# Performance work log

Measured on AMD Instinct MI355X. Metric: run time of the kernel, lower is better.

The kernel has to match this reference:

```python
import jax, jax.numpy as jnp
import numpy as np

N_NODES = 100000
N_EDGES = 800000
N_FEAT = 128
N_HID = 128
N_LAYERS = 3
N_CLASSES = 10
N_GRAPHS = 256


def setup_inputs() -> dict:
    key = jax.random.key(0)
    ks = jax.random.split(key, 6)
    x = jax.random.normal(ks[0], (N_NODES, N_FEAT), dtype=jnp.float32)
    edge_index = jax.random.randint(ks[1], (2, N_EDGES), 0, N_NODES, dtype=jnp.int64)
    batch = jnp.sort(jax.random.randint(ks[2], (N_NODES,), 0, N_GRAPHS, dtype=jnp.int64))
    # GCNConv weights: layer 0 is [num_feature, num_hidden], rest [hid, hid];
    # num_feature == num_hidden here so we stack them as [L, H, H].
    Ws = jax.random.normal(ks[3], (N_LAYERS, N_HID, N_HID), dtype=jnp.float32) * 0.05
    bs = jnp.zeros((N_LAYERS, N_HID), dtype=jnp.float32)
    Wc = jax.random.normal(ks[4], (N_HID, N_CLASSES), dtype=jnp.float32) * 0.05
    bc = jnp.zeros((N_CLASSES,), dtype=jnp.float32)
    return {"x": x, "edge_index": edge_index, "batch": batch,
            "Ws": Ws, "bs": bs, "Wc": Wc, "bc": bc}


def reference(x, edge_index, batch, Ws, bs, Wc, bc):
    n = x.shape[0]
    # PyG GCNConv: add self-loops, symmetric normalization deg^{-1/2} A deg^{-1/2}
    loop = jnp.arange(n, dtype=edge_index.dtype)
    src = jnp.concatenate([edge_index[0], loop])  # [E+N]
    dst = jnp.concatenate([edge_index[1], loop])
    deg = jax.ops.segment_sum(jnp.ones_like(src, dtype=x.dtype), dst, num_segments=n)
    dinv = jax.lax.rsqrt(deg)  # deg >= 1 due to self-loops
    norm = dinv[src] * dinv[dst]  # [E+N]

    for l in range(N_LAYERS):
        h = x @ Ws[l]  # [N, H] dense transform
        msgs = h[src] * norm[:, None]  # gather + scale, [E+N, H]
        x = jax.ops.segment_sum(msgs, dst, num_segments=n) + bs[l]
        x = jax.nn.elu(x)
        # F.dropout(training=self.training): identity in eval mode

    g = jax.ops.segment_max(x, batch, num_segments=N_GRAPHS)  # global_max_pool [G, H]
    logits = g @ Wc + bc
    return jax.nn.softmax(logits, axis=1)
```

## Files before the change

kernel.cpp:

```cpp
#include <hip/hip_runtime.h>
#include <float.h>
#include <math.h>

#define NNODES 100000
#define NEDGES 800000
#define NF 128
#define NCLASSES 10
#define NGRAPHS 256

#define NBIN 98
#define BCHUNK 4096
#define NB2 196
#define CNTS_PAD 20480
#define SCAN_CHUNK 2048

typedef __attribute__((ext_vector_type(8))) short bf16x8;
typedef __attribute__((ext_vector_type(4))) float f32x4;

__device__ inline ushort f2bf(float f) {
    unsigned u = __float_as_uint(f);
    u = u + 0x7FFFu + ((u >> 16) & 1u);
    return (ushort)(u >> 16);
}
__device__ inline float b2f(ushort h) {
    return __uint_as_float(((unsigned)h) << 16);
}
__device__ inline void up2(unsigned u, float& lo, float& hi) {
    lo = __uint_as_float(u << 16);
    hi = __uint_as_float(u & 0xFFFF0000u);
}
__device__ inline unsigned fenc(float f) {
    unsigned u = __float_as_uint(f);
    return ((int)u < 0) ? ~u : (u | 0x80000000u);
}
__device__ inline float fdec(unsigned s) {
    return (s & 0x80000000u) ? __uint_as_float(s ^ 0x80000000u) : __uint_as_float(~s);
}

__global__ __launch_bounds__(256) void binct_kernel(const int* __restrict__ dst,
                                                    unsigned* __restrict__ cnts, int E) {
    __shared__ unsigned lh[NBIN];
    int tid = threadIdx.x;
    if (tid < NBIN) lh[tid] = 0;
    __syncthreads();
    int e0 = blockIdx.x * BCHUNK;
    int e1 = min(e0 + BCHUNK, E);
    for (int e = e0 + tid; e < e1; e += 256)
        atomicAdd(&lh[dst[e] >> 10], 1u);
    __syncthreads();
    if (tid < NBIN) cnts[tid * NB2 + blockIdx.x] = lh[tid];
}

__global__ __launch_bounds__(256) void scanA_kernel(const unsigned* __restrict__ cnt,
                                                    unsigned* __restrict__ bsum, int N) {
    __shared__ unsigned wsum[4];
    int tid = threadIdx.x, wid = tid >> 6, lane = tid & 63;
    int base = blockIdx.x * SCAN_CHUNK + tid * 8;
    unsigned s = 0;
    if (base < N) {
        uint4 a = *(const uint4*)(cnt + base);
        uint4 b = *(const uint4*)(cnt + base + 4);
        s = a.x + a.y + a.z + a.w + b.x + b.y + b.z + b.w;
    }
    #pragma unroll
    for (int off = 32; off >= 1; off >>= 1) s += __shfl_down(s, off, 64);
    if (lane == 0) wsum[wid] = s;
    __syncthreads();
    if (tid == 0) bsum[blockIdx.x] = wsum[0] + wsum[1] + wsum[2] + wsum[3];
}

__global__ __launch_bounds__(64) void scanB_kernel(const unsigned* __restrict__ bsum,
                                                   unsigned* __restrict__ boff, int nb) {
    int lane = threadIdx.x;
    unsigned v = (lane < nb) ? bsum[lane] : 0u;
    unsigned incl = v;
    #pragma unroll
    for (int off = 1; off < 64; off <<= 1) {
        unsigned t = __shfl_up(incl, off, 64);
        if (lane >= off) incl += t;
    }
    if (lane < nb) boff[lane] = incl - v;
}

__global__ __launch_bounds__(256) void scanC_kernel(const unsigned* __restrict__ cnt,
                                                    const unsigned* __restrict__ boff,
                                                    unsigned* __restrict__ outp, int N) {
    __shared__ unsigned wsum[4];
    int tid = threadIdx.x, wid = tid >> 6, lane = tid & 63;
    int base = blockIdx.x * SCAN_CHUNK + tid * 8;
    unsigned v[8];
    unsigned s = 0;
    bool act = base < N;
    if (act) {
        uint4 a = *(const uint4*)(cnt + base);
        uint4 b = *(const uint4*)(cnt + base + 4);
        v[0] = a.x; v[1] = a.y; v[2] = a.z; v[3] = a.w;
        v[4] = b.x; v[5] = b.y; v[6] = b.z; v[7] = b.w;
        #pragma unroll
        for (int j = 0; j < 8; ++j) s += v[j];
    }
    unsigned incl = s;
    #pragma unroll
    for (int off = 1; off < 64; off <<= 1) {
        unsigned t = __shfl_up(incl, off, 64);
        if (lane >= off) incl += t;
    }
    if (lane == 63) wsum[wid] = incl;
    __syncthreads();
    unsigned woff = 0;
    for (int w = 0; w < 4; ++w) if (w < wid) woff += wsum[w];
    if (act) {
        unsigned run = incl - s + woff + boff[blockIdx.x];
        #pragma unroll
        for (int j = 0; j < 8; ++j) {
            outp[base + j] = run;
            run += v[j];
        }
    }
}

__global__ __launch_bounds__(256) void binscatter_kernel(const int* __restrict__ src,
                                                         const int* __restrict__ dst,
                                                         const unsigned* __restrict__ offs,
                                                         unsigned* __restrict__ bedge, int E) {
    __shared__ unsigned lcur[NBIN];
    int tid = threadIdx.x;
    if (tid < NBIN) lcur[tid] = offs[tid * NB2 + blockIdx.x];
    __syncthreads();
    int e0 = blockIdx.x * BCHUNK;
    int e1 = min(e0 + BCHUNK, E);
    for (int e = e0 + tid; e < e1; e += 256) {
        int d = dst[e];
        int b = d >> 10;
        unsigned pos = atomicAdd(&lcur[b], 1u);
        bedge[pos] = ((unsigned)src[e] << 10) | (unsigned)(d & 1023);
    }
}

__global__ __launch_bounds__(256) void bucket_kernel(const unsigned* __restrict__ bedge,
                                                     const unsigned* __restrict__ offs,
                                                     float* __restrict__ dinv,
                                                     unsigned* __restrict__ rowptr,
                                                     unsigned* __restrict__ csr_src, int N) {
    __shared__ unsigned lcnt[1024];
    __shared__ unsigned lcur[1024];
    __shared__ unsigned wsum[4];
    int b = blockIdx.x;
    int tid = threadIdx.x, wid = tid >> 6, lane = tid & 63;
    unsigned ebeg = offs[b * NB2], eend = offs[(b + 1) * NB2];
    lcnt[tid] = 0; lcnt[tid + 256] = 0; lcnt[tid + 512] = 0; lcnt[tid + 768] = 0;
    __syncthreads();
    for (unsigned e = ebeg + tid; e < eend; e += 256)
        atomicAdd(&lcnt[bedge[e] & 1023], 1u);
    __syncthreads();
    unsigned c[4];
    unsigned s = 0;
    #pragma unroll
    for (int j = 0; j < 4; ++j) { c[j] = lcnt[tid * 4 + j]; s += c[j]; }
    unsigned incl = s;
    #pragma unroll
    for (int off = 1; off < 64; off <<= 1) {
        unsigned t = __shfl_up(incl, off, 64);
        if (lane >= off) incl += t;
    }
    if (lane == 63) wsum[wid] = incl;
    __syncthreads();
    unsigned woff = 0;
    for (int w = 0; w < 4; ++w) if (w < wid) woff += wsum[w];
    unsigned run = (incl - s) + woff + ebeg;
    int gbase = b * 1024 + tid * 4;
    #pragma unroll
    for (int j = 0; j < 4; ++j) {
        if (gbase + j < N) {
            rowptr[gbase + j] = run;
            dinv[gbase + j] = rsqrtf((float)c[j] + 1.0f);
        }
        lcur[tid * 4 + j] = run;
        run += c[j];
    }
    if (b == NBIN - 1 && tid == 0) rowptr[N] = eend;
    __syncthreads();
    for (unsigned e = ebeg + tid; e < eend; e += 256) {
        unsigned v = bedge[e];
        unsigned pos = atomicAdd(&lcur[v & 1023], 1u);
        csr_src[pos] = v >> 10;
    }
}

__global__ __launch_bounds__(256) void wprep_kernel(const float* __restrict__ Ws,
                                                    short* __restrict__ Wf) {
    int l = blockIdx.x;
    for (int idx = threadIdx.x; idx < 16384; idx += 256) {
        int i = idx & 7;
        int lane = (idx >> 3) & 63;
        int ns = idx >> 9;
        int s = ns & 3, nt = ns >> 2;
        int k = s * 32 + (lane >> 4) * 8 + i;
        int n = nt * 16 + (lane & 15);
        Wf[l * 16384 + idx] = (short)f2bf(Ws[l * 16384 + k * NF + n]);
    }
}

template<bool L0>
__global__ __launch_bounds__(256) void gemm_mfma_kernel(const void* __restrict__ Xin,
                                                        const short* __restrict__ Wf,
                                                        ushort* __restrict__ Hb, int M) {
    __shared__ short Wl[16384];
    int tid = threadIdx.x;
    for (int i = tid; i < 2048; i += 256)
        ((float4*)Wl)[i] = ((const float4*)Wf)[i];

    int wave = tid >> 6, lane = tid & 63;
    int r = lane & 15, kg = lane >> 4;
    int rowbase = blockIdx.x * 128 + wave * 32;

    bf16x8 afrag[2][4];
    #pragma unroll
    for (int t = 0; t < 2; ++t) {
        #pragma unroll
        for (int s = 0; s < 4; ++s) {
            int row = rowbase + t * 16 + r;
            if (row > M - 1) row = M - 1;
            if (L0) {
                const float* p = (const float*)Xin + (size_t)row * NF + s * 32 + kg * 8;
                float4 u0 = *(const float4*)p;
                float4 u1 = *(const float4*)(p + 4);
                bf16x8 a;
                a[0] = (short)f2bf(u0.x); a[1] = (short)f2bf(u0.y);
                a[2] = (short)f2bf(u0.z); a[3] = (short)f2bf(u0.w);
                a[4] = (short)f2bf(u1.x); a[5] = (short)f2bf(u1.y);
                a[6] = (short)f2bf(u1.z); a[7] = (short)f2bf(u1.w);
                afrag[t][s] = a;
            } else {
                afrag[t][s] = *(const bf16x8*)((const ushort*)Xin + (size_t)row * NF + s * 32 + kg * 8);
            }
        }
    }

    f32x4 acc[2][8];
    #pragma unroll
    for (int t = 0; t < 2; ++t)
        #pragma unroll
        for (int n = 0; n < 8; ++n)
            acc[t][n] = (f32x4){0.f, 0.f, 0.f, 0.f};

    __syncthreads();
    const bf16x8* WL = (const bf16x8*)Wl;
    #pragma unroll
    for (int s = 0; s < 4; ++s) {
        #pragma unroll
        for (int n = 0; n < 8; ++n) {
            bf16x8 bfr = WL[(n * 4 + s) * 64 + lane];
            acc[0][n] = __builtin_amdgcn_mfma_f32_16x16x32_bf16(afrag[0][s], bfr, acc[0][n], 0, 0, 0);
            acc[1][n] = __builtin_amdgcn_mfma_f32_16x16x32_bf16(afrag[1][s], bfr, acc[1][n], 0, 0, 0);
        }
    }

    __syncthreads();
    ushort* Cl = (ushort*)Wl;
    int r4 = kg * 4;
    #pragma unroll
    for (int t = 0; t < 2; ++t) {
        #pragma unroll
        for (int n = 0; n < 8; ++n) {
            #pragma unroll
            for (int q = 0; q < 4; ++q) {
                Cl[(wave * 32 + t * 16 + r4 + q) * NF + n * 16 + r] = f2bf(acc[t][n][q]);
            }
        }
    }
    __syncthreads();
    int row0 = blockIdx.x * 128;
    #pragma unroll
    for (int k = 0; k < 8; ++k) {
        int c = k * 256 + tid;
        int row = row0 + (c >> 4);
        if (row < M)
            ((uint4*)Hb)[(size_t)row * 16 + (c & 15)] = ((const uint4*)Cl)[c];
    }
}

__global__ __launch_bounds__(256) void aggregate_kernel(const ushort* __restrict__ Hb,
                                                        const float* __restrict__ dinv,
                                                        const unsigned* __restrict__ rowptr,
                                                        const unsigned* __restrict__ csr_src,
                                                        const float* __restrict__ bias,
                                                        ushort* __restrict__ Xout, int N) {
    int gid = blockIdx.x * 256 + threadIdx.x;
    int node = gid >> 4;
    int lane = gid & 15;
    int c0 = lane * 8;
    float di = dinv[node];
    float sl = di * di;
    float4 b0 = ((const float4*)bias)[lane * 2 + 0];
    float4 b1 = ((const float4*)bias)[lane * 2 + 1];
    uint4 hv = *(const uint4*)(Hb + (size_t)node * NF + c0);
    float a0, a1, a2, a3, a4, a5, a6, a7, t0, t1;
    up2(hv.x, t0, t1); a0 = fmaf(t0, sl, b0.x); a1 = fmaf(t1, sl, b0.y);
    up2(hv.y, t0, t1); a2 = fmaf(t0, sl, b0.z); a3 = fmaf(t1, sl, b0.w);
    up2(hv.z, t0, t1); a4 = fmaf(t0, sl, b1.x); a5 = fmaf(t1, sl, b1.y);
    up2(hv.w, t0, t1); a6 = fmaf(t0, sl, b1.z); a7 = fmaf(t1, sl, b1.w);
    unsigned e = rowptr[node], end = rowptr[node + 1];
    for (; e + 4 <= end; e += 4) {
        unsigned s0 = csr_src[e + 0], s1 = csr_src[e + 1];
        unsigned s2 = csr_src[e + 2], s3 = csr_src[e + 3];
        float n0 = dinv[s0] * di, n1 = dinv[s1] * di;
        float n2 = dinv[s2] * di, n3 = dinv[s3] * di;
        uint4 g0 = *(const uint4*)(Hb + (size_t)s0 * NF + c0);
        uint4 g1 = *(const uint4*)(Hb + (size_t)s1 * NF + c0);
        uint4 g2 = *(const uint4*)(Hb + (size_t)s2 * NF + c0);
        uint4 g3 = *(const uint4*)(Hb + (size_t)s3 * NF + c0);
        up2(g0.x, t0, t1); a0 = fmaf(t0, n0, a0); a1 = fmaf(t1, n0, a1);
        up2(g0.y, t0, t1); a2 = fmaf(t0, n0, a2); a3 = fmaf(t1, n0, a3);
        up2(g0.z, t0, t1); a4 = fmaf(t0, n0, a4); a5 = fmaf(t1, n0, a5);
        up2(g0.w, t0, t1); a6 = fmaf(t0, n0, a6); a7 = fmaf(t1, n0, a7);
        up2(g1.x, t0, t1); a0 = fmaf(t0, n1, a0); a1 = fmaf(t1, n1, a1);
        up2(g1.y, t0, t1); a2 = fmaf(t0, n1, a2); a3 = fmaf(t1, n1, a3);
        up2(g1.z, t0, t1); a4 = fmaf(t0, n1, a4); a5 = fmaf(t1, n1, a5);
        up2(g1.w, t0, t1); a6 = fmaf(t0, n1, a6); a7 = fmaf(t1, n1, a7);
        up2(g2.x, t0, t1); a0 = fmaf(t0, n2, a0); a1 = fmaf(t1, n2, a1);
        up2(g2.y, t0, t1); a2 = fmaf(t0, n2, a2); a3 = fmaf(t1, n2, a3);
        up2(g2.z, t0, t1); a4 = fmaf(t0, n2, a4); a5 = fmaf(t1, n2, a5);
        up2(g2.w, t0, t1); a6 = fmaf(t0, n2, a6); a7 = fmaf(t1, n2, a7);
        up2(g3.x, t0, t1); a0 = fmaf(t0, n3, a0); a1 = fmaf(t1, n3, a1);
        up2(g3.y, t0, t1); a2 = fmaf(t0, n3, a2); a3 = fmaf(t1, n3, a3);
        up2(g3.z, t0, t1); a4 = fmaf(t0, n3, a4); a5 = fmaf(t1, n3, a5);
        up2(g3.w, t0, t1); a6 = fmaf(t0, n3, a6); a7 = fmaf(t1, n3, a7);
    }
    for (; e < end; ++e) {
        unsigned s = csr_src[e];
        float nm = dinv[s] * di;
        uint4 g = *(const uint4*)(Hb + (size_t)s * NF + c0);
        up2(g.x, t0, t1); a0 = fmaf(t0, nm, a0); a1 = fmaf(t1, nm, a1);
        up2(g.y, t0, t1); a2 = fmaf(t0, nm, a2); a3 = fmaf(t1, nm, a3);
        up2(g.z, t0, t1); a4 = fmaf(t0, nm, a4); a5 = fmaf(t1, nm, a5);
        up2(g.w, t0, t1); a6 = fmaf(t0, nm, a6); a7 = fmaf(t1, nm, a7);
    }
    a0 = a0 > 0.f ? a0 : expm1f(a0);
    a1 = a1 > 0.f ? a1 : expm1f(a1);
    a2 = a2 > 0.f ? a2 : expm1f(a2);
    a3 = a3 > 0.f ? a3 : expm1f(a3);
    a4 = a4 > 0.f ? a4 : expm1f(a4);
    a5 = a5 > 0.f ? a5 : expm1f(a5);
    a6 = a6 > 0.f ? a6 : expm1f(a6);
    a7 = a7 > 0.f ? a7 : expm1f(a7);
    uint4 o;
    o.x = ((unsigned)f2bf(a1) << 16) | f2bf(a0);
    o.y = ((unsigned)f2bf(a3) << 16) | f2bf(a2);
    o.z = ((unsigned)f2bf(a5) << 16) | f2bf(a4);
    o.w = ((unsigned)f2bf(a7) << 16) | f2bf(a6);
    *(uint4*)(Xout + (size_t)node * NF + c0) = o;
}

__global__ __launch_bounds__(256) void aggregate_pool_kernel(const ushort* __restrict__ Hb,
                                                             const float* __restrict__ dinv,
                                                             const unsigned* __restrict__ rowptr,
                                                             const unsigned* __restrict__ csr_src,
                                                             const float* __restrict__ bias,
                                                             const int* __restrict__ batch,
                                                             unsigned* __restrict__ Gx, int N) {
    __shared__ unsigned lmax[16][NF];
    __shared__ int g0s;
    int tid = threadIdx.x;
    int gid = blockIdx.x * 256 + tid;
    int node = gid >> 4;
    int lane = gid & 15;
    int c0 = lane * 8;
    for (int i = tid; i < 16 * NF; i += 256) ((unsigned*)lmax)[i] = 0;
    if (tid == 0) g0s = batch[blockIdx.x * 16];
    __syncthreads();
    float di = dinv[node];
    float sl = di * di;
    float4 b0 = ((const float4*)bias)[lane * 2 + 0];
    float4 b1 = ((const float4*)bias)[lane * 2 + 1];
    uint4 hv = *(const uint4*)(Hb + (size_t)node * NF + c0);
    float a0, a1, a2, a3, a4, a5, a6, a7, t0, t1;
    up2(hv.x, t0, t1); a0 = fmaf(t0, sl, b0.x); a1 = fmaf(t1, sl, b0.y);
    up2(hv.y, t0, t1); a2 = fmaf(t0, sl, b0.z); a3 = fmaf(t1, sl, b0.w);
    up2(hv.z, t0, t1); a4 = fmaf(t0, sl, b1.x); a5 = fmaf(t1, sl, b1.y);
    up2(hv.w, t0, t1); a6 = fmaf(t0, sl, b1.z); a7 = fmaf(t1, sl, b1.w);
    unsigned e = rowptr[node], end = rowptr[node + 1];
    for (; e + 4 <= end; e += 4) {
        unsigned s0 = csr_src[e + 0], s1 = csr_src[e + 1];
        unsigned s2 = csr_src[e + 2], s3 = csr_src[e + 3];
        float n0 = dinv[s0] * di, n1 = dinv[s1] * di;
        float n2 = dinv[s2] * di, n3 = dinv[s3] * di;
        uint4 g0 = *(const uint4*)(Hb + (size_t)s0 * NF + c0);
        uint4 g1 = *(const uint4*)(Hb + (size_t)s1 * NF + c0);
        uint4 g2 = *(const uint4*)(Hb + (size_t)s2 * NF + c0);
        uint4 g3 = *(const uint4*)(Hb + (size_t)s3 * NF + c0);
        up2(g0.x, t0, t1); a0 = fmaf(t0, n0, a0); a1 = fmaf(t1, n0, a1);
        up2(g0.y, t0, t1); a2 = fmaf(t0, n0, a2); a3 = fmaf(t1, n0, a3);
        up2(g0.z, t0, t1); a4 = fmaf(t0, n0, a4); a5 = fmaf(t1, n0, a5);
        up2(g0.w, t0, t1); a6 = fmaf(t0, n0, a6); a7 = fmaf(t1, n0, a7);
        up2(g1.x, t0, t1); a0 = fmaf(t0, n1, a0); a1 = fmaf(t1, n1, a1);
        up2(g1.y, t0, t1); a2 = fmaf(t0, n1, a2); a3 = fmaf(t1, n1, a3);
        up2(g1.z, t0, t1); a4 = fmaf(t0, n1, a4); a5 = fmaf(t1, n1, a5);
        up2(g1.w, t0, t1); a6 = fmaf(t0, n1, a6); a7 = fmaf(t1, n1, a7);
        up2(g2.x, t0, t1); a0 = fmaf(t0, n2, a0); a1 = fmaf(t1, n2, a1);
        up2(g2.y, t0, t1); a2 = fmaf(t0, n2, a2); a3 = fmaf(t1, n2, a3);
        up2(g2.z, t0, t1); a4 = fmaf(t0, n2, a4); a5 = fmaf(t1, n2, a5);
        up2(g2.w, t0, t1); a6 = fmaf(t0, n2, a6); a7 = fmaf(t1, n2, a7);
        up2(g3.x, t0, t1); a0 = fmaf(t0, n3, a0); a1 = fmaf(t1, n3, a1);
        up2(g3.y, t0, t1); a2 = fmaf(t0, n3, a2); a3 = fmaf(t1, n3, a3);
        up2(g3.z, t0, t1); a4 = fmaf(t0, n3, a4); a5 = fmaf(t1, n3, a5);
        up2(g3.w, t0, t1); a6 = fmaf(t0, n3, a6); a7 = fmaf(t1, n3, a7);
    }
    for (; e < end; ++e) {
        unsigned s = csr_src[e];
        float nm = dinv[s] * di;
        uint4 g = *(const uint4*)(Hb + (size_t)s * NF + c0);
        up2(g.x, t0, t1); a0 = fmaf(t0, nm, a0); a1 = fmaf(t1, nm, a1);
        up2(g.y, t0, t1); a2 = fmaf(t0, nm, a2); a3 = fmaf(t1, nm, a3);
        up2(g.z, t0, t1); a4 = fmaf(t0, nm, a4); a5 = fmaf(t1, nm, a5);
        up2(g.w, t0, t1); a6 = fmaf(t0, nm, a6); a7 = fmaf(t1, nm, a7);
    }
    a0 = a0 > 0.f ? a0 : expm1f(a0);
    a1 = a1 > 0.f ? a1 : expm1f(a1);
    a2 = a2 > 0.f ? a2 : expm1f(a2);
    a3 = a3 > 0.f ? a3 : expm1f(a3);
    a4 = a4 > 0.f ? a4 : expm1f(a4);
    a5 = a5 > 0.f ? a5 : expm1f(a5);
    a6 = a6 > 0.f ? a6 : expm1f(a6);
    a7 = a7 > 0.f ? a7 : expm1f(a7);
    int slot = batch[node] - g0s;
    unsigned* lm = &lmax[slot][c0];
    atomicMax(lm + 0, fenc(a0)); atomicMax(lm + 1, fenc(a1));
    atomicMax(lm + 2, fenc(a2)); atomicMax(lm + 3, fenc(a3));
    atomicMax(lm + 4, fenc(a4)); atomicMax(lm + 5, fenc(a5));
    atomicMax(lm + 6, fenc(a6)); atomicMax(lm + 7, fenc(a7));
    __syncthreads();
    for (int i = tid; i < 16 * NF; i += 256) {
        unsigned v = ((unsigned*)lmax)[i];
        if (v) atomicMax(&Gx[(size_t)(g0s + (i >> 7)) * NF + (i & (NF - 1))], v);
    }
}

__global__ __launch_bounds__(128) void classify_kernel(const unsigned* __restrict__ Gx,
                                                       const float* __restrict__ Wc,
                                                       const float* __restrict__ bc,
                                                       float* __restrict__ out) {
    __shared__ float gr[NF];
    __shared__ float lg[NCLASSES];
    int g = blockIdx.x;
    int tid = threadIdx.x;
    gr[tid] = fdec(Gx[(size_t)g * NF + tid]);
    __syncthreads();
    if (tid < NCLASSES) {
        float s = bc[tid];
        for (int k = 0; k < NF; ++k) s = fmaf(gr[k], Wc[k * NCLASSES + tid], s);
        lg[tid] = s;
    }
    __syncthreads();
    if (tid == 0) {
        float m = lg[0];
        #pragma unroll
        for (int c = 1; c < NCLASSES; ++c) m = fmaxf(m, lg[c]);
        float e[NCLASSES];
        float sum = 0.f;
        #pragma unroll
        for (int c = 0; c < NCLASSES; ++c) { e[c] = expf(lg[c] - m); sum += e[c]; }
        #pragma unroll
        for (int c = 0; c < NCLASSES; ++c) out[g * NCLASSES + c] = e[c] / sum;
    }
}

extern "C" void kernel_launch(void* const* d_in, const int* in_sizes, int n_in,
                              void* d_out, int out_size, void* d_ws, size_t ws_size,
                              hipStream_t stream) {
    const float* x     = (const float*)d_in[0];
    const int*   ei    = (const int*)d_in[1];
    const int*   batch = (const int*)d_in[2];
    const float* Ws    = (const float*)d_in[3];
    const float* bs    = (const float*)d_in[4];
    const float* Wc    = (const float*)d_in[5];
    const float* bc    = (const float*)d_in[6];
    float* out = (float*)d_out;

    const int* src = ei;
    const int* dst = ei + NEDGES;

    char* ws = (char*)d_ws;
    size_t off = 0;
    auto alloc = [&](size_t bytes) -> void* {
        off = (off + 255) & ~(size_t)255;
        void* p = ws + off;
        off += bytes;
        return p;
    };
    ushort*   B0      = (ushort*)alloc(sizeof(ushort) * (size_t)NNODES * NF);
    ushort*   B1      = (ushort*)alloc(sizeof(ushort) * (size_t)NNODES * NF);
    ushort*   Hb      = (ushort*)alloc(sizeof(ushort) * (size_t)NNODES * NF);
    float*    dinvp   = (float*)alloc(sizeof(float) * NNODES);
    unsigned* rowptr  = (unsigned*)alloc(sizeof(unsigned) * (NNODES + 1));
    unsigned* csr_src = (unsigned*)alloc(sizeof(unsigned) * NEDGES);
    unsigned* bedge   = (unsigned*)alloc(sizeof(unsigned) * NEDGES);
    unsigned* offs    = (unsigned*)alloc(sizeof(unsigned) * (CNTS_PAD + 1));
    unsigned* bsum    = (unsigned*)alloc(sizeof(unsigned) * 16);
    unsigned* boff    = (unsigned*)alloc(sizeof(unsigned) * 16);
    short*    Wf      = (short*)alloc(sizeof(short) * 3 * 16384);
    unsigned* cnts    = (unsigned*)alloc(sizeof(unsigned) * CNTS_PAD);
    unsigned* Gx      = (unsigned*)alloc(sizeof(unsigned) * NGRAPHS * NF);
    size_t zspan = (size_t)((char*)(Gx + NGRAPHS * NF) - (char*)cnts);

    hipMemsetAsync(cnts, 0, zspan, stream);
    wprep_kernel<<<3, 256, 0, stream>>>(Ws, Wf);
    binct_kernel<<<NB2, 256, 0, stream>>>(dst, cnts, NEDGES);
    scanA_kernel<<<CNTS_PAD / SCAN_CHUNK, 256, 0, stream>>>(cnts, bsum, CNTS_PAD);
    scanB_kernel<<<1, 64, 0, stream>>>(bsum, boff, CNTS_PAD / SCAN_CHUNK);
    scanC_kernel<<<CNTS_PAD / SCAN_CHUNK, 256, 0, stream>>>(cnts, boff, offs, CNTS_PAD);
    binscatter_kernel<<<NB2, 256, 0, stream>>>(src, dst, offs, bedge, NEDGES);
    bucket_kernel<<<NBIN, 256, 0, stream>>>(bedge, offs, dinvp, rowptr, csr_src, NNODES);

    int gemm_grid = (NNODES + 127) / 128;
    int agg_grid  = NNODES / 16;

    gemm_mfma_kernel<true><<<gemm_grid, 256, 0, stream>>>(x, Wf + 0 * 16384, Hb, NNODES);
    aggregate_kernel<<<agg_grid, 256, 0, stream>>>(Hb, dinvp, rowptr, csr_src,
                                                   bs + 0 * NF, B1, NNODES);
    gemm_mfma_kernel<false><<<gemm_grid, 256, 0, stream>>>(B1, Wf + 1 * 16384, Hb, NNODES);
    aggregate_kernel<<<agg_grid, 256, 0, stream>>>(Hb, dinvp, rowptr, csr_src,
                                                   bs + 1 * NF, B0, NNODES);
    gemm_mfma_kernel<false><<<gemm_grid, 256, 0, stream>>>(B0, Wf + 2 * 16384, Hb, NNODES);
    aggregate_pool_kernel<<<agg_grid, 256, 0, stream>>>(Hb, dinvp, rowptr, csr_src,
                                                        bs + 2 * NF, batch, Gx, NNODES);

    classify_kernel<<<NGRAPHS, 128, 0, stream>>>(Gx, Wc, bc, out);
}
```

Before: 232.2 us.

## Fuse aggregation with next layer's GEMM via shared-memory staging

Merges the aggregate kernel for layers 0 and 1 with the following MFMA GEMM into one 512-thread kernel. Each block aggregates 128 nodes into an XOR-swizzled LDS tile and then multiplies it by the next weight matrix, so the intermediate activation buffers are no longer written to and re-read from global memory. This also removes two kernel launches. In exchange the larger LDS footprint (about 64 KB per block) may lower occupancy, and the gather latency now sits in the same block as the GEMM phase.

```diff
diff --git a/kernel.cpp b/kernel.cpp
--- a/kernel.cpp
+++ b/kernel.cpp
@@ -201,10 +201,9 @@
     }
 }
 
-template<bool L0>
-__global__ __launch_bounds__(256) void gemm_mfma_kernel(const void* __restrict__ Xin,
-                                                        const short* __restrict__ Wf,
-                                                        ushort* __restrict__ Hb, int M) {
+__global__ __launch_bounds__(256) void gemm_l0_kernel(const float* __restrict__ Xin,
+                                                      const short* __restrict__ Wf,
+                                                      ushort* __restrict__ Hb, int M) {
     __shared__ short Wl[16384];
     int tid = threadIdx.x;
     for (int i = tid; i < 2048; i += 256)
@@ -221,19 +220,15 @@
         for (int s = 0; s < 4; ++s) {
             int row = rowbase + t * 16 + r;
             if (row > M - 1) row = M - 1;
-            if (L0) {
-                const float* p = (const float*)Xin + (size_t)row * NF + s * 32 + kg * 8;
-                float4 u0 = *(const float4*)p;
-                float4 u1 = *(const float4*)(p + 4);
-                bf16x8 a;
-                a[0] = (short)f2bf(u0.x); a[1] = (short)f2bf(u0.y);
-                a[2] = (short)f2bf(u0.z); a[3] = (short)f2bf(u0.w);
-                a[4] = (short)f2bf(u1.x); a[5] = (short)f2bf(u1.y);
-                a[6] = (short)f2bf(u1.z); a[7] = (short)f2bf(u1.w);
-                afrag[t][s] = a;
-            } else {
-                afrag[t][s] = *(const bf16x8*)((const ushort*)Xin + (size_t)row * NF + s * 32 + kg * 8);
-            }
+            const float* p = Xin + (size_t)row * NF + s * 32 + kg * 8;
+            float4 u0 = *(const float4*)p;
+            float4 u1 = *(const float4*)(p + 4);
+            bf16x8 a;
+            a[0] = (short)f2bf(u0.x); a[1] = (short)f2bf(u0.y);
+            a[2] = (short)f2bf(u0.z); a[3] = (short)f2bf(u0.w);
+            a[4] = (short)f2bf(u1.x); a[5] = (short)f2bf(u1.y);
+            a[6] = (short)f2bf(u1.z); a[7] = (short)f2bf(u1.w);
+            afrag[t][s] = a;
         }
     }
 
@@ -280,16 +275,150 @@
     }
 }
 
-__global__ __launch_bounds__(256) void aggregate_kernel(const ushort* __restrict__ Hb,
-                                                        const float* __restrict__ dinv,
-                                                        const unsigned* __restrict__ rowptr,
-                                                        const unsigned* __restrict__ csr_src,
-                                                        const float* __restrict__ bias,
-                                                        ushort* __restrict__ Xout, int N) {
-    int gid = blockIdx.x * 256 + threadIdx.x;
+__global__ __launch_bounds__(512) void fused_agg_gemm_kernel(const ushort* __restrict__ Hin,
+                                                             const float* __restrict__ dinv,
+                                                             const unsigned* __restrict__ rowptr,
+                                                             const unsigned* __restrict__ csr_src,
+                                                             const float* __restrict__ bias,
+                                                             const short* __restrict__ Wf,
+                                                             ushort* __restrict__ Hout, int M) {
+    __shared__ short Wl[16384];
+    __shared__ uint4 Xl4[128][16];
+
+    int tid = threadIdx.x;
+    for (int i = tid; i < 2048; i += 512)
+        ((float4*)Wl)[i] = ((const float4*)Wf)[i];
+
+    int lane16 = tid & 15;
+    int c0 = lane16 * 8;
+    float4 b0 = ((const float4*)bias)[lane16 * 2 + 0];
+    float4 b1 = ((const float4*)bias)[lane16 * 2 + 1];
+    #pragma unroll
+    for (int it = 0; it < 4; ++it) {
+        int row = it * 32 + (tid >> 4);
+        int node = blockIdx.x * 128 + row;
+        uint4 o = make_uint4(0u, 0u, 0u, 0u);
+        if (node < M) {
+            float di = dinv[node];
+            float sl = di * di;
+            uint4 hv = *(const uint4*)(Hin + (size_t)node * NF + c0);
+            float a0, a1, a2, a3, a4, a5, a6, a7, t0, t1;
+            up2(hv.x, t0, t1); a0 = fmaf(t0, sl, b0.x); a1 = fmaf(t1, sl, b0.y);
+            up2(hv.y, t0, t1); a2 = fmaf(t0, sl, b0.z); a3 = fmaf(t1, sl, b0.w);
+            up2(hv.z, t0, t1); a4 = fmaf(t0, sl, b1.x); a5 = fmaf(t1, sl, b1.y);
+            up2(hv.w, t0, t1); a6 = fmaf(t0, sl, b1.z); a7 = fmaf(t1, sl, b1.w);
+            unsigned e = rowptr[node], end = rowptr[node + 1];
+            for (; e + 4 <= end; e += 4) {
+                unsigned s0 = csr_src[e + 0], s1 = csr_src[e + 1];
+                unsigned s2 = csr_src[e + 2], s3 = csr_src[e + 3];
+                float n0 = dinv[s0] * di, n1 = dinv[s1] * di;
+                float n2 = dinv[s2] * di, n3 = dinv[s3] * di;
+                uint4 g0 = *(const uint4*)(Hin + (size_t)s0 * NF + c0);
+                uint4 g1 = *(const uint4*)(Hin + (size_t)s1 * NF + c0);
+                uint4 g2 = *(const uint4*)(Hin + (size_t)s2 * NF + c0);
+                uint4 g3 = *(const uint4*)(Hin + (size_t)s3 * NF + c0);
+                up2(g0.x, t0, t1); a0 = fmaf(t0, n0, a0); a1 = fmaf(t1, n0, a1);
+                up2(g0.y, t0, t1); a2 = fmaf(t0, n0, a2); a3 = fmaf(t1, n0, a3);
+                up2(g0.z, t0, t1); a4 = fmaf(t0, n0, a4); a5 = fmaf(t1, n0, a5);
+                up2(g0.w, t0, t1); a6 = fmaf(t0, n0, a6); a7 = fmaf(t1, n0, a7);
+                up2(g1.x, t0, t1); a0 = fmaf(t0, n1, a0); a1 = fmaf(t1, n1, a1);
+                up2(g1.y, t0, t1); a2 = fmaf(t0, n1, a2); a3 = fmaf(t1, n1, a3);
+                up2(g1.z, t0, t1); a4 = fmaf(t0, n1, a4); a5 = fmaf(t1, n1, a5);
+                up2(g1.w, t0, t1); a6 = fmaf(t0, n1, a6); a7 = fmaf(t1, n1, a7);
+                up2(g2.x, t0, t1); a0 = fmaf(t0, n2, a0); a1 = fmaf(t1, n2, a1);
+                up2(g2.y, t0, t1); a2 = fmaf(t0, n2, a2); a3 = fmaf(t1, n2, a3);
+                up2(g2.z, t0, t1); a4 = fmaf(t0, n2, a4); a5 = fmaf(t1, n2, a5);
+                up2(g2.w, t0, t1); a6 = fmaf(t0, n2, a6); a7 = fmaf(t1, n2, a7);
+                up2(g3.x, t0, t1); a0 = fmaf(t0, n3, a0); a1 = fmaf(t1, n3, a1);
+                up2(g3.y, t0, t1); a2 = fmaf(t0, n3, a2); a3 = fmaf(t1, n3, a3);
+                up2(g3.z, t0, t1); a4 = fmaf(t0, n3, a4); a5 = fmaf(t1, n3, a5);
+                up2(g3.w, t0, t1); a6 = fmaf(t0, n3, a6); a7 = fmaf(t1, n3, a7);
+            }
+            for (; e < end; ++e) {
+                unsigned s = csr_src[e];
+                float nm = dinv[s] * di;
+                uint4 g = *(const uint4*)(Hin + (size_t)s * NF + c0);
+                up2(g.x, t0, t1); a0 = fmaf(t0, nm, a0); a1 = fmaf(t1, nm, a1);
+                up2(g.y, t0, t1); a2 = fmaf(t0, nm, a2); a3 = fmaf(t1, nm, a3);
+                up2(g.z, t0, t1); a4 = fmaf(t0, nm, a4); a5 = fmaf(t1, nm, a5);
+                up2(g.w, t0, t1); a6 = fmaf(t0, nm, a6); a7 = fmaf(t1, nm, a7);
+            }
+            a0 = a0 > 0.f ? a0 : expm1f(a0);
+            a1 = a1 > 0.f ? a1 : expm1f(a1);
+            a2 = a2 > 0.f ? a2 : expm1f(a2);
+            a3 = a3 > 0.f ? a3 : expm1f(a3);
+            a4 = a4 > 0.f ? a4 : expm1f(a4);
+            a5 = a5 > 0.f ? a5 : expm1f(a5);
+            a6 = a6 > 0.f ? a6 : expm1f(a6);
+            a7 = a7 > 0.f ? a7 : expm1f(a7);
+            o.x = ((unsigned)f2bf(a1) << 16) | f2bf(a0);
+            o.y = ((unsigned)f2bf(a3) << 16) | f2bf(a2);
+            o.z = ((unsigned)f2bf(a5) << 16) | f2bf(a4);
+            o.w = ((unsigned)f2bf(a7) << 16) | f2bf(a6);
+        }
+        Xl4[row][lane16 ^ (row & 15)] = o;
+    }
+    __syncthreads();
+
+    int wave = tid >> 6, lane = tid & 63;
+    int r = lane & 15, kg = lane >> 4;
+    int rl = wave * 16 + r;
+    bf16x8 afrag[4];
+    #pragma unroll
+    for (int s = 0; s < 4; ++s)
+        afrag[s] = *(const bf16x8*)&Xl4[rl][(s * 4 + kg) ^ r];
+    __syncthreads();
+
+    f32x4 acc[8];
+    #pragma unroll
+    for (int n = 0; n < 8; ++n) acc[n] = (f32x4){0.f, 0.f, 0.f, 0.f};
+    const bf16x8* WL = (const bf16x8*)Wl;
+    #pragma unroll
+    for (int s = 0; s < 4; ++s) {
+        #pragma unroll
+        for (int n = 0; n < 8; ++n) {
+            bf16x8 bfr = WL[(n * 4 + s) * 64 + lane];
+            acc[n] = __builtin_amdgcn_mfma_f32_16x16x32_bf16(afrag[s], bfr, acc[n], 0, 0, 0);
+        }
+    }
+
+    ushort* Cl = (ushort*)Xl4;
+    int r4 = kg * 4;
+    #pragma unroll
+    for (int n = 0; n < 8; ++n) {
+        #pragma unroll
+        for (int q = 0; q < 4; ++q) {
+            Cl[(wave * 16 + r4 + q) * NF + n * 16 + r] = f2bf(acc[n][q]);
+        }
+    }
+    __syncthreads();
+    int row0 = blockIdx.x * 128;
+    #pragma unroll
+    for (int k = 0; k < 4; ++k) {
+        int c = k * 512 + tid;
+        int row = row0 + (c >> 4);
+        if (row < M)
+            ((uint4*)Hout)[(size_t)row * 16 + (c & 15)] = ((const uint4*)Cl)[c];
+    }
+}
+
+__global__ __launch_bounds__(256) void aggregate_pool_kernel(const ushort* __restrict__ Hb,
+                                                             const float* __restrict__ dinv,
+                                                             const unsigned* __restrict__ rowptr,
+                                                             const unsigned* __restrict__ csr_src,
+                                                             const float* __restrict__ bias,
+                                                             const int* __restrict__ batch,
+                                                             unsigned* __restrict__ Gx, int N) {
+    __shared__ unsigned lmax[16][NF];
+    __shared__ int g0s;
+    int tid = threadIdx.x;
+    int gid = blockIdx.x * 256 + tid;
     int node = gid >> 4;
     int lane = gid & 15;
     int c0 = lane * 8;
+    for (int i = tid; i < 16 * NF; i += 256) ((unsigned*)lmax)[i] = 0;
+    if (tid == 0) g0s = batch[blockIdx.x * 16];
+    __syncthreads();
     float di = dinv[node];
     float sl = di * di;
     float4 b0 = ((const float4*)bias)[lane * 2 + 0];
@@ -344,85 +473,6 @@
     a5 = a5 > 0.f ? a5 : expm1f(a5);
     a6 = a6 > 0.f ? a6 : expm1f(a6);
     a7 = a7 > 0.f ? a7 : expm1f(a7);
-    uint4 o;
-    o.x = ((unsigned)f2bf(a1) << 16) | f2bf(a0);
-    o.y = ((unsigned)f2bf(a3) << 16) | f2bf(a2);
-    o.z = ((unsigned)f2bf(a5) << 16) | f2bf(a4);
-    o.w = ((unsigned)f2bf(a7) << 16) | f2bf(a6);
-    *(uint4*)(Xout + (size_t)node * NF + c0) = o;
-}
-
-__global__ __launch_bounds__(256) void aggregate_pool_kernel(const ushort* __restrict__ Hb,
-                                                             const float* __restrict__ dinv,
-                                                             const unsigned* __restrict__ rowptr,
-                                                             const unsigned* __restrict__ csr_src,
-                                                             const float* __restrict__ bias,
-                                                             const int* __restrict__ batch,
-                                                             unsigned* __restrict__ Gx, int N) {
-    __shared__ unsigned lmax[16][NF];
-    __shared__ int g0s;
-    int tid = threadIdx.x;
-    int gid = blockIdx.x * 256 + tid;
-    int node = gid >> 4;
-    int lane = gid & 15;
-    int c0 = lane * 8;
-    for (int i = tid; i < 16 * NF; i += 256) ((unsigned*)lmax)[i] = 0;
-    if (tid == 0) g0s = batch[blockIdx.x * 16];
-    __syncthreads();
-    float di = dinv[node];
-    float sl = di * di;
-    float4 b0 = ((const float4*)bias)[lane * 2 + 0];
-    float4 b1 = ((const float4*)bias)[lane * 2 + 1];
-    uint4 hv = *(const uint4*)(Hb + (size_t)node * NF + c0);
-    float a0, a1, a2, a3, a4, a5, a6, a7, t0, t1;
-    up2(hv.x, t0, t1); a0 = fmaf(t0, sl, b0.x); a1 = fmaf(t1, sl, b0.y);
-    up2(hv.y, t0, t1); a2 = fmaf(t0, sl, b0.z); a3 = fmaf(t1, sl, b0.w);
-    up2(hv.z, t0, t1); a4 = fmaf(t0, sl, b1.x); a5 = fmaf(t1, sl, b1.y);
-    up2(hv.w, t0, t1); a6 = fmaf(t0, sl, b1.z); a7 = fmaf(t1, sl, b1.w);
-    unsigned e = rowptr[node], end = rowptr[node + 1];
-    for (; e + 4 <= end; e += 4) {
-        unsigned s0 = csr_src[e + 0], s1 = csr_src[e + 1];
-        unsigned s2 = csr_src[e + 2], s3 = csr_src[e + 3];
-        float n0 = dinv[s0] * di, n1 = dinv[s1] * di;
-        float n2 = dinv[s2] * di, n3 = dinv[s3] * di;
-        uint4 g0 = *(const uint4*)(Hb + (size_t)s0 * NF + c0);
-        uint4 g1 = *(const uint4*)(Hb + (size_t)s1 * NF + c0);
-        uint4 g2 = *(const uint4*)(Hb + (size_t)s2 * NF + c0);
-        uint4 g3 = *(const uint4*)(Hb + (size_t)s3 * NF + c0);
-        up2(g0.x, t0, t1); a0 = fmaf(t0, n0, a0); a1 = fmaf(t1, n0, a1);
-        up2(g0.y, t0, t1); a2 = fmaf(t0, n0, a2); a3 = fmaf(t1, n0, a3);
-        up2(g0.z, t0, t1); a4 = fmaf(t0, n0, a4); a5 = fmaf(t1, n0, a5);
-        up2(g0.w, t0, t1); a6 = fmaf(t0, n0, a6); a7 = fmaf(t1, n0, a7);
-        up2(g1.x, t0, t1); a0 = fmaf(t0, n1, a0); a1 = fmaf(t1, n1, a1);
-        up2(g1.y, t0, t1); a2 = fmaf(t0, n1, a2); a3 = fmaf(t1, n1, a3);
-        up2(g1.z, t0, t1); a4 = fmaf(t0, n1, a4); a5 = fmaf(t1, n1, a5);
-        up2(g1.w, t0, t1); a6 = fmaf(t0, n1, a6); a7 = fmaf(t1, n1, a7);
-        up2(g2.x, t0, t1); a0 = fmaf(t0, n2, a0); a1 = fmaf(t1, n2, a1);
-        up2(g2.y, t0, t1); a2 = fmaf(t0, n2, a2); a3 = fmaf(t1, n2, a3);
-        up2(g2.z, t0, t1); a4 = fmaf(t0, n2, a4); a5 = fmaf(t1, n2, a5);
-        up2(g2.w, t0, t1); a6 = fmaf(t0, n2, a6); a7 = fmaf(t1, n2, a7);
-        up2(g3.x, t0, t1); a0 = fmaf(t0, n3, a0); a1 = fmaf(t1, n3, a1);
-        up2(g3.y, t0, t1); a2 = fmaf(t0, n3, a2); a3 = fmaf(t1, n3, a3);
-        up2(g3.z, t0, t1); a4 = fmaf(t0, n3, a4); a5 = fmaf(t1, n3, a5);
-        up2(g3.w, t0, t1); a6 = fmaf(t0, n3, a6); a7 = fmaf(t1, n3, a7);
-    }
-    for (; e < end; ++e) {
-        unsigned s = csr_src[e];
-        float nm = dinv[s] * di;
-        uint4 g = *(const uint4*)(Hb + (size_t)s * NF + c0);
-        up2(g.x, t0, t1); a0 = fmaf(t0, nm, a0); a1 = fmaf(t1, nm, a1);
-        up2(g.y, t0, t1); a2 = fmaf(t0, nm, a2); a3 = fmaf(t1, nm, a3);
-        up2(g.z, t0, t1); a4 = fmaf(t0, nm, a4); a5 = fmaf(t1, nm, a5);
-        up2(g.w, t0, t1); a6 = fmaf(t0, nm, a6); a7 = fmaf(t1, nm, a7);
-    }
-    a0 = a0 > 0.f ? a0 : expm1f(a0);
-    a1 = a1 > 0.f ? a1 : expm1f(a1);
-    a2 = a2 > 0.f ? a2 : expm1f(a2);
-    a3 = a3 > 0.f ? a3 : expm1f(a3);
-    a4 = a4 > 0.f ? a4 : expm1f(a4);
-    a5 = a5 > 0.f ? a5 : expm1f(a5);
-    a6 = a6 > 0.f ? a6 : expm1f(a6);
-    a7 = a7 > 0.f ? a7 : expm1f(a7);
     int slot = batch[node] - g0s;
     unsigned* lm = &lmax[slot][c0];
     atomicMax(lm + 0, fenc(a0)); atomicMax(lm + 1, fenc(a1));
@@ -488,9 +538,8 @@
         off += bytes;
         return p;
     };
-    ushort*   B0      = (ushort*)alloc(sizeof(ushort) * (size_t)NNODES * NF);
-    ushort*   B1      = (ushort*)alloc(sizeof(ushort) * (size_t)NNODES * NF);
     ushort*   Hb      = (ushort*)alloc(sizeof(ushort) * (size_t)NNODES * NF);
+    ushort*   Hb2     = (ushort*)alloc(sizeof(ushort) * (size_t)NNODES * NF);
     float*    dinvp   = (float*)alloc(sizeof(float) * NNODES);
     unsigned* rowptr  = (unsigned*)alloc(sizeof(unsigned) * (NNODES + 1));
     unsigned* csr_src = (unsigned*)alloc(sizeof(unsigned) * NEDGES);
@@ -515,13 +564,11 @@
     int gemm_grid = (NNODES + 127) / 128;
     int agg_grid  = NNODES / 16;
 
-    gemm_mfma_kernel<true><<<gemm_grid, 256, 0, stream>>>(x, Wf + 0 * 16384, Hb, NNODES);
-    aggregate_kernel<<<agg_grid, 256, 0, stream>>>(Hb, dinvp, rowptr, csr_src,
-                                                   bs + 0 * NF, B1, NNODES);
-    gemm_mfma_kernel<false><<<gemm_grid, 256, 0, stream>>>(B1, Wf + 1 * 16384, Hb, NNODES);
-    aggregate_kernel<<<agg_grid, 256, 0, stream>>>(Hb, dinvp, rowptr, csr_src,
-                                                   bs + 1 * NF, B0, NNODES);
-    gemm_mfma_kernel<false><<<gemm_grid, 256, 0, stream>>>(B0, Wf + 2 * 16384, Hb, NNODES);
+    gemm_l0_kernel<<<gemm_grid, 256, 0, stream>>>(x, Wf + 0 * 16384, Hb, NNODES);
+    fused_agg_gemm_kernel<<<gemm_grid, 512, 0, stream>>>(Hb, dinvp, rowptr, csr_src,
+                                                         bs + 0 * NF, Wf + 1 * 16384, Hb2, NNODES);
+    fused_agg_gemm_kernel<<<gemm_grid, 512, 0, stream>>>(Hb2, dinvp, rowptr, csr_src,
+                                                         bs + 1 * NF, Wf + 2 * 16384, Hb, NNODES);
     aggregate_pool_kernel<<<agg_grid, 256, 0, stream>>>(Hb, dinvp, rowptr, csr_src,
                                                         bs + 2 * NF, batch, Gx, NNODES);
 
```

After: 242.2 us. 4.3% more time.
